# Kernel tuning notes

Hardware: AMD Instinct MI355X
Metric: run time of the kernel (lower is better)

The kernel has to match this reference:

```python
import jax, jax.numpy as jnp
import numpy as np

UNITS = [100, 80, 50, 30]
D_IN = 64


def _lstm_layer(x, Wx, Wh, b):
    # x: [B, T, D]; Wx: [D, 4u]; Wh: [u, 4u]; b: [4u]
    B = x.shape[0]
    u = Wh.shape[0]
    # precompute input contribution for all timesteps: [B, T, 4u]
    xg = jnp.einsum('btd,dg->btg', x, Wx) + b

    def step(carry, xg_t):
        h, c = carry
        g = xg_t + h @ Wh                      # [B, 4u]
        i, f, cbar, o = jnp.split(g, 4, axis=-1)
        i = jax.nn.sigmoid(i)
        f = jax.nn.sigmoid(f)
        o = jax.nn.sigmoid(o)
        c = f * c + i * jnp.tanh(cbar)
        h = o * jnp.tanh(c)
        return (h, c), h

    init = (jnp.zeros((B, u), x.dtype), jnp.zeros((B, u), x.dtype))
    (h_final, _), hs = jax.lax.scan(step, init, jnp.swapaxes(xg, 0, 1))
    return jnp.swapaxes(hs, 0, 1), h_final  # [B, T, u], [B, u]


def setup_inputs() -> dict:
    key = jax.random.key(0)
    ks = jax.random.split(key, 16)
    B, T = 256, 1024
    inp = {"sequence": jax.random.normal(ks[0], (B, T, D_IN), dtype=jnp.float32)}
    d_in = D_IN
    for li, u in enumerate(UNITS):
        s_x = 1.0 / np.sqrt(d_in)
        s_h = 1.0 / np.sqrt(u)
        inp[f"Wx{li}"] = jax.random.normal(ks[1 + 3 * li], (d_in, 4 * u), dtype=jnp.float32) * s_x
        inp[f"Wh{li}"] = jax.random.normal(ks[2 + 3 * li], (u, 4 * u), dtype=jnp.float32) * s_h
        inp[f"b{li}"] = jnp.zeros((4 * u,), dtype=jnp.float32)
        d_in = u
    inp["W_out"] = jax.random.normal(ks[13], (UNITS[-1], 1), dtype=jnp.float32) / np.sqrt(UNITS[-1])
    inp["b_out"] = jnp.zeros((1,), dtype=jnp.float32)
    return inp


def reference(sequence, Wx0, Wh0, b0, Wx1, Wh1, b1, Wx2, Wh2, b2, Wx3, Wh3, b3, W_out, b_out):
    # 4 stacked LSTM layers; dropout is identity at inference.
    x, _ = _lstm_layer(sequence, Wx0, Wh0, b0)   # [B, T, 100]
    x, _ = _lstm_layer(x, Wx1, Wh1, b1)          # [B, T, 80]
    x, _ = _lstm_layer(x, Wx2, Wh2, b2)          # [B, T, 50]
    _, h = _lstm_layer(x, Wx3, Wh3, b3)          # final state [B, 30]
    return h @ W_out + b_out                     # [B, 1]
```

## Files before the change

kernel.cpp:

```cpp
#include <hip/hip_runtime.h>


#define BATCH 256
#define TFULL 1024
#define TC    64
#define NCHUNK (TFULL / TC)
#define NDIAG  (NCHUNK + 3)

__device__ __forceinline__ float fast_rcp(float x) {
    return __builtin_amdgcn_rcpf(x);
}

__device__ __forceinline__ float tanh_fast(float x) {
    float e = __expf(-2.0f * fabsf(x));
    float r = fast_rcp(1.0f + e);
    return copysignf(fmaf(2.0f, r, -1.0f), x);
}

__device__ __forceinline__ void lds_barrier() {
    asm volatile("s_waitcnt lgkmcnt(0)\n\ts_barrier" ::: "memory");
}

template<int CTRL>
__device__ __forceinline__ float dpp_add(float v) {
    int t = __builtin_amdgcn_update_dpp(0, __float_as_int(v), CTRL, 0xF, 0xF, true);
    return v + __int_as_float(t);
}
template<int CTRL>
__device__ __forceinline__ float dpp_mov(float v) {
    int t = __builtin_amdgcn_update_dpp(0, __float_as_int(v), CTRL, 0xF, 0xF, true);
    return __int_as_float(t);
}

template<int K, int N>
__device__ __forceinline__ void gemm_body(
    const float* __restrict__ x, int batchStride,
    const float* __restrict__ Wx,
    const float* __restrict__ bias,
    float* __restrict__ out,
    int lid, float* __restrict__ smem)
{
    constexpr int K4   = (K + 3) / 4;
    constexpr int SLAB = 64 * 4 + 4;
    constexpr int GX   = (N + 63) / 64;

    float* s_A = smem;
    float* s_B = smem + K4 * SLAB;

    const int n0   = (lid % GX) * 64;
    const int row0 = (lid / GX) * 64;
    const int tid  = threadIdx.x;
    const int tx   = tid & 15;
    const int ty   = tid >> 4;

    if constexpr ((K % 4) == 0) {
        for (int i = tid; i < 64 * (K / 4); i += 256) {
            const int row = i / (K / 4);
            const int k4  = i % (K / 4);
            const int gr  = row0 + row;
            const int b   = gr >> 6;
            const int t   = gr & 63;
            float4 v = *(const float4*)(x + (size_t)b * batchStride + t * K + k4 * 4);
            *(float4*)(s_A + k4 * SLAB + row * 4) = v;
        }
    } else {
        for (int i = tid; i < 64 * K; i += 256) {
            const int row = i / K;
            const int k   = i % K;
            const int gr  = row0 + row;
            const int b   = gr >> 6;
            const int t   = gr & 63;
            s_A[(k >> 2) * SLAB + row * 4 + (k & 3)] =
                x[(size_t)b * batchStride + t * K + k];
        }
        constexpr int PAD = K4 * 4 - K;
        for (int i = tid; i < 64 * PAD; i += 256) {
            const int row = i / PAD;
            const int kk  = K + i % PAD;
            s_A[(kk >> 2) * SLAB + row * 4 + (kk & 3)] = 0.0f;
        }
    }

    for (int i = tid; i < K4 * 4 * 16; i += 256) {
        const int k  = i >> 4;
        const int c4 = i & 15;
        float4 v = {0.0f, 0.0f, 0.0f, 0.0f};
        if (k < K && n0 + c4 * 4 < N)
            v = *(const float4*)(Wx + (size_t)k * N + n0 + c4 * 4);
        *(float4*)(s_B + k * 64 + c4 * 4) = v;
    }
    __syncthreads();

    float acc[4][4];
#pragma unroll
    for (int r = 0; r < 4; ++r)
#pragma unroll
        for (int c = 0; c < 4; ++c) acc[r][c] = 0.0f;

    for (int k4 = 0; k4 < K4; ++k4) {
        float4 bv[4];
#pragma unroll
        for (int j = 0; j < 4; ++j)
            bv[j] = *(const float4*)(s_B + (k4 * 4 + j) * 64 + tx * 4);
#pragma unroll
        for (int r = 0; r < 4; ++r) {
            float4 av = *(const float4*)(s_A + k4 * SLAB + (ty + 16 * r) * 4);
#pragma unroll
            for (int c = 0; c < 4; ++c) {
                acc[r][c] = fmaf(av.x, ((const float*)&bv[0])[c], acc[r][c]);
                acc[r][c] = fmaf(av.y, ((const float*)&bv[1])[c], acc[r][c]);
                acc[r][c] = fmaf(av.z, ((const float*)&bv[2])[c], acc[r][c]);
                acc[r][c] = fmaf(av.w, ((const float*)&bv[3])[c], acc[r][c]);
            }
        }
    }

    if (n0 + tx * 4 < N) {
        float4 bb = *(const float4*)(bias + n0 + tx * 4);
#pragma unroll
        for (int r = 0; r < 4; ++r) {
            float4 o;
            o.x = acc[r][0] + bb.x;
            o.y = acc[r][1] + bb.y;
            o.z = acc[r][2] + bb.z;
            o.w = acc[r][3] + bb.w;
            *(float4*)(out + (size_t)(row0 + ty + 16 * r) * N + n0 + tx * 4) = o;
        }
    }
}

struct GemmArgs {
    const float *x0, *x1, *x2, *x3;
    float *o0, *o1, *o2, *o3;
    const float *Wx0, *bi0, *Wx1, *bi1, *Wx2, *bi2, *Wx3, *bi3;
    int off1, off2, off3;
};

__global__ __launch_bounds__(256, 2)
void xg_all(GemmArgs a)
{
    __shared__ __align__(16) float smem[12900];
    const int bid = blockIdx.x;
    if (bid < a.off1)
        gemm_body<64, 400>(a.x0, TFULL * 64, a.Wx0, a.bi0, a.o0, bid, smem);
    else if (bid < a.off2)
        gemm_body<100, 320>(a.x1, TC * 100, a.Wx1, a.bi1, a.o1, bid - a.off1, smem);
    else if (bid < a.off3)
        gemm_body<80, 200>(a.x2, TC * 80, a.Wx2, a.bi2, a.o2, bid - a.off2, smem);
    else
        gemm_body<50, 120>(a.x3, TC * 50, a.Wx3, a.bi3, a.o3, bid - a.off3, smem);
}

template<int U, int S, int BLOCK, bool LAST>
__device__ __forceinline__ void rec4_body(
    float* __restrict__ s_h,
    const float* __restrict__ xg,
    const float* __restrict__ Wh,
    float* __restrict__ xout,
    float* __restrict__ c_state,
    float* __restrict__ h_state,
    int first, int b,
    const float* __restrict__ Wout,
    const float* __restrict__ bout,
    float* __restrict__ dout)
{
    constexpr int G  = 4 * U;
    constexpr int HS = 4 * S;

    const int tid = threadIdx.x;
    const int u   = tid >> 2;
    const int s   = tid & 3;
    const bool act_th = (u < U);
    const int uu  = act_th ? u : 0;
    const bool wave_act = ((tid & ~63) < 4 * U);

    float w4[4][S];
#pragma unroll
    for (int g = 0; g < 4; ++g)
#pragma unroll
        for (int kk = 0; kk < S; ++kk) {
            const int k = s * S + kk;
            w4[g][kk] = (act_th && k < U) ? Wh[(size_t)k * G + g * U + uu] : 0.0f;
        }

    for (int i = tid; i < 2 * HS; i += BLOCK) s_h[i] = 0.0f;
    __syncthreads();
    if (tid < U) s_h[tid] = first ? 0.0f : h_state[b * U + tid];
    float c = first ? 0.0f : c_state[b * U + uu];
    __syncthreads();

    const float* xgp = xg + (size_t)b * TC * G + (s * U + uu);
    float xg0 = xgp[0];
    float xg1 = xgp[G];

    int cur = 0;
    float h = 0.0f, hprev = 0.0f;
    const bool is_t = (s == 2);

    for (int t = 0; t < TC; ++t, cur ^= 1) {
        if (wave_act) {
            const int tp = (t + 2 < TC) ? (t + 2) : (TC - 1);
            const float xg2 = xgp[(size_t)tp * G];

            if (!LAST) {
                if (act_th && s == 0 && t > 0)
                    xout[((size_t)b * TC + (t - 1)) * U + u] = hprev;
            }

            float a0 = 0.0f, a1 = 0.0f, a2 = 0.0f, a3 = 0.0f;
            const float* hs = s_h + cur * HS + s * S;
#pragma unroll
            for (int kk = 0; kk < S; kk += 4) {
                float4 v = *(const float4*)(hs + kk);
                a0 = fmaf(v.x, w4[0][kk + 0], a0);
                a0 = fmaf(v.y, w4[0][kk + 1], a0);
                a0 = fmaf(v.z, w4[0][kk + 2], a0);
                a0 = fmaf(v.w, w4[0][kk + 3], a0);
                a1 = fmaf(v.x, w4[1][kk + 0], a1);
                a1 = fmaf(v.y, w4[1][kk + 1], a1);
                a1 = fmaf(v.z, w4[1][kk + 2], a1);
                a1 = fmaf(v.w, w4[1][kk + 3], a1);
                a2 = fmaf(v.x, w4[2][kk + 0], a2);
                a2 = fmaf(v.y, w4[2][kk + 1], a2);
                a2 = fmaf(v.z, w4[2][kk + 2], a2);
                a2 = fmaf(v.w, w4[2][kk + 3], a2);
                a3 = fmaf(v.x, w4[3][kk + 0], a3);
                a3 = fmaf(v.y, w4[3][kk + 1], a3);
                a3 = fmaf(v.z, w4[3][kk + 2], a3);
                a3 = fmaf(v.w, w4[3][kk + 3], a3);
            }

            a0 = dpp_add<0xB1>(a0); a0 = dpp_add<0x4E>(a0);
            a1 = dpp_add<0xB1>(a1); a1 = dpp_add<0x4E>(a1);
            a2 = dpp_add<0xB1>(a2); a2 = dpp_add<0x4E>(a2);
            a3 = dpp_add<0xB1>(a3); a3 = dpp_add<0x4E>(a3);

            const float asum = (s == 0) ? a0 : (s == 1) ? a1 : (s == 2) ? a2 : a3;
            const float gs = asum + xg0;
            const float y  = is_t ? (-2.0f * fabsf(gs)) : (-gs);
            const float r  = fast_rcp(1.0f + __expf(y));
            const float v  = is_t ? copysignf(fmaf(2.0f, r, -1.0f), gs) : r;

            const float fi = dpp_mov<0x00>(v);
            const float ff = dpp_mov<0x55>(v);
            const float tc = dpp_mov<0xAA>(v);
            const float fo = dpp_mov<0xFF>(v);
            c = fmaf(ff, c, fi * tc);
            h = fo * tanh_fast(c);

            const int nxt = cur ^ 1;
            if (act_th && s == 0) s_h[nxt * HS + u] = h;
            hprev = h;
            xg0 = xg1; xg1 = xg2;
        }
        lds_barrier();
    }

    if (!LAST) {
        if (act_th && s == 0)
            xout[((size_t)b * TC + (TC - 1)) * U + u] = hprev;
    }
    if (act_th && s == 0) {
        c_state[b * U + u] = c;
        h_state[b * U + u] = h;
    }
    if (LAST && tid == 0) {
        float acc = bout[0];
#pragma unroll
        for (int k = 0; k < U; ++k) acc = fmaf(s_h[cur * HS + k], Wout[k], acc);
        dout[b] = acc;
    }
}

struct RecArgs {
    const float *xg0, *xg1, *xg2, *xg3;
    const float *Wh0, *Wh1, *Wh2, *Wh3;
    float *xc0, *xc1, *xc2;
    float *c0, *h0, *c1, *h1, *c2, *h2, *c3, *h3;
    const float *Wout, *bout;
    float *dout;
    int d;
};

__global__ __attribute__((amdgpu_flat_work_group_size(448, 448),
                          amdgpu_waves_per_eu(4, 8)))
void rec_all(RecArgs a)
{
    __shared__ __align__(16) float s_h[2 * 112];
    const int grp = blockIdx.x >> 8;
    const int b   = blockIdx.x & 255;
    const int j   = a.d - grp;
    if (j < 0 || j >= NCHUNK) return;
    const int first = (j == 0) ? 1 : 0;
    switch (grp) {
    case 0: rec4_body<100, 28, 448, false>(s_h, a.xg0, a.Wh0, a.xc0, a.c0, a.h0,
                                           first, b, nullptr, nullptr, nullptr); break;
    case 1: rec4_body< 80, 20, 448, false>(s_h, a.xg1, a.Wh1, a.xc1, a.c1, a.h1,
                                           first, b, nullptr, nullptr, nullptr); break;
    case 2: rec4_body< 50, 16, 448, false>(s_h, a.xg2, a.Wh2, a.xc2, a.c2, a.h2,
                                           first, b, nullptr, nullptr, nullptr); break;
    default: rec4_body< 30,  8, 448, true >(s_h, a.xg3, a.Wh3, nullptr, a.c3, a.h3,
                                           first, b, a.Wout, a.bout, a.dout); break;
    }
}

extern "C" void kernel_launch(void* const* d_in, const int* in_sizes, int n_in,
                              void* d_out, int out_size, void* d_ws, size_t ws_size,
                              hipStream_t stream)
{
    const float* seq  = (const float*)d_in[0];
    const float* Wx0  = (const float*)d_in[1];
    const float* Wh0  = (const float*)d_in[2];
    const float* b0   = (const float*)d_in[3];
    const float* Wx1  = (const float*)d_in[4];
    const float* Wh1  = (const float*)d_in[5];
    const float* b1   = (const float*)d_in[6];
    const float* Wx2  = (const float*)d_in[7];
    const float* Wh2  = (const float*)d_in[8];
    const float* b2   = (const float*)d_in[9];
    const float* Wx3  = (const float*)d_in[10];
    const float* Wh3  = (const float*)d_in[11];
    const float* b3   = (const float*)d_in[12];
    const float* Wout = (const float*)d_in[13];
    const float* bout = (const float*)d_in[14];
    float* out = (float*)d_out;

    float* ws  = (float*)d_ws;
    float* XG0 = ws;
    float* XG1 = XG0 + (size_t)BATCH * TC * 400;
    float* XG2 = XG1 + (size_t)BATCH * TC * 320;
    float* XG3 = XG2 + (size_t)BATCH * TC * 200;
    float* XC0 = XG3 + (size_t)BATCH * TC * 120;
    float* XC1 = XC0 + (size_t)BATCH * TC * 100;
    float* XC2 = XC1 + (size_t)BATCH * TC * 80;
    float* st  = XC2 + (size_t)BATCH * TC * 50;
    float* sc0 = st + 0 * 32768; float* sh0 = st + 1 * 32768;
    float* sc1 = st + 2 * 32768; float* sh1 = st + 3 * 32768;
    float* sc2 = st + 4 * 32768; float* sh2 = st + 5 * 32768;
    float* sc3 = st + 6 * 32768; float* sh3 = st + 7 * 32768;

    const int NB0 = 7 * 256, NB1 = 5 * 256, NB2 = 4 * 256, NB3 = 2 * 256;

    for (int d = 0; d < NDIAG; ++d) {
        GemmArgs ga;
        ga.x0 = nullptr; ga.x1 = nullptr; ga.x2 = nullptr; ga.x3 = nullptr;
        ga.o0 = XG0; ga.o1 = XG1; ga.o2 = XG2; ga.o3 = XG3;
        ga.Wx0 = Wx0; ga.bi0 = b0; ga.Wx1 = Wx1; ga.bi1 = b1;
        ga.Wx2 = Wx2; ga.bi2 = b2; ga.Wx3 = Wx3; ga.bi3 = b3;
        int nb = 0;
        if (d < NCHUNK)                { ga.x0 = seq + (size_t)d * TC * 64; nb += NB0; }
        ga.off1 = nb;
        if (d >= 1 && d - 1 < NCHUNK)  { ga.x1 = XC0; nb += NB1; }
        ga.off2 = nb;
        if (d >= 2 && d - 2 < NCHUNK)  { ga.x2 = XC1; nb += NB2; }
        ga.off3 = nb;
        if (d >= 3 && d - 3 < NCHUNK)  { ga.x3 = XC2; nb += NB3; }

        xg_all<<<dim3(nb), dim3(256), 0, stream>>>(ga);

        RecArgs ra;
        ra.xg0 = XG0; ra.xg1 = XG1; ra.xg2 = XG2; ra.xg3 = XG3;
        ra.Wh0 = Wh0; ra.Wh1 = Wh1; ra.Wh2 = Wh2; ra.Wh3 = Wh3;
        ra.xc0 = XC0; ra.xc1 = XC1; ra.xc2 = XC2;
        ra.c0 = sc0; ra.h0 = sh0; ra.c1 = sc1; ra.h1 = sh1;
        ra.c2 = sc2; ra.h2 = sh2; ra.c3 = sc3; ra.h3 = sh3;
        ra.Wout = Wout; ra.bout = bout; ra.dout = out;
        ra.d = d;

        rec_all<<<dim3(4 * 256), dim3(448), 0, stream>>>(ra);
    }
}
```

Baseline: 2.880 ms.

## Use fp16 MFMA for recurrent matmul, batching 16 sequences per block

The recurrent step moves from a per-sequence scalar FMA dot product (one block per batch element) to a 16-row MFMA tile. Each block now processes 16 sequences with Wh held in registers as fp16 fragments, and h is stored in LDS as fp16. The gate columns of the xg GEMM output are interleaved (i,f,c,o per unit) so each unit's four gates land in adjacent lanes for the DPP gather. The launch shrinks from 1024 blocks to 64 blocks of 512 threads. This trades precision (fp16 h and Wh) and parallelism (fewer blocks) for far fewer per-step instructions.

```diff
diff --git a/kernel.cpp b/kernel.cpp
--- a/kernel.cpp
+++ b/kernel.cpp
@@ -1,4 +1,5 @@
 #include <hip/hip_runtime.h>
+#include <hip/hip_fp16.h>
 
 
 #define BATCH 256
@@ -7,6 +8,9 @@
 #define NCHUNK (TFULL / TC)
 #define NDIAG  (NCHUNK + 3)
 
+typedef __attribute__((ext_vector_type(8))) _Float16 f16x8;
+typedef __attribute__((ext_vector_type(4))) float    f32x4;
+
 __device__ __forceinline__ float fast_rcp(float x) {
     return __builtin_amdgcn_rcpf(x);
 }
@@ -21,11 +25,6 @@
     asm volatile("s_waitcnt lgkmcnt(0)\n\ts_barrier" ::: "memory");
 }
 
-template<int CTRL>
-__device__ __forceinline__ float dpp_add(float v) {
-    int t = __builtin_amdgcn_update_dpp(0, __float_as_int(v), CTRL, 0xF, 0xF, true);
-    return v + __int_as_float(t);
-}
 template<int CTRL>
 __device__ __forceinline__ float dpp_mov(float v) {
     int t = __builtin_amdgcn_update_dpp(0, __float_as_int(v), CTRL, 0xF, 0xF, true);
@@ -43,6 +42,7 @@
     constexpr int K4   = (K + 3) / 4;
     constexpr int SLAB = 64 * 4 + 4;
     constexpr int GX   = (N + 63) / 64;
+    constexpr int U    = N / 4;
 
     float* s_A = smem;
     float* s_B = smem + K4 * SLAB;
@@ -84,9 +84,15 @@
     for (int i = tid; i < K4 * 4 * 16; i += 256) {
         const int k  = i >> 4;
         const int c4 = i & 15;
+        const int base = n0 + c4 * 4;
         float4 v = {0.0f, 0.0f, 0.0f, 0.0f};
-        if (k < K && n0 + c4 * 4 < N)
-            v = *(const float4*)(Wx + (size_t)k * N + n0 + c4 * 4);
+        if (k < K && base < N) {
+            const int q = base >> 2;
+            v.x = Wx[(size_t)k * N + 0 * U + q];
+            v.y = Wx[(size_t)k * N + 1 * U + q];
+            v.z = Wx[(size_t)k * N + 2 * U + q];
+            v.w = Wx[(size_t)k * N + 3 * U + q];
+        }
         *(float4*)(s_B + k * 64 + c4 * 4) = v;
     }
     __syncthreads();
@@ -116,7 +122,12 @@
     }
 
     if (n0 + tx * 4 < N) {
-        float4 bb = *(const float4*)(bias + n0 + tx * 4);
+        const int q = (n0 + tx * 4) >> 2;
+        float4 bb;
+        bb.x = bias[0 * U + q];
+        bb.y = bias[1 * U + q];
+        bb.z = bias[2 * U + q];
+        bb.w = bias[3 * U + q];
 #pragma unroll
         for (int r = 0; r < 4; ++r) {
             float4 o;
@@ -151,124 +162,162 @@
         gemm_body<50, 120>(a.x3, TC * 50, a.Wx3, a.bi3, a.o3, bid - a.off3, smem);
 }
 
-template<int U, int S, int BLOCK, bool LAST>
-__device__ __forceinline__ void rec4_body(
-    float* __restrict__ s_h,
+template<int U, int NT, int KT, bool LAST>
+__device__ __forceinline__ void recm_body(
     const float* __restrict__ xg,
     const float* __restrict__ Wh,
     float* __restrict__ xout,
     float* __restrict__ c_state,
     float* __restrict__ h_state,
-    int first, int b,
-    const float* __restrict__ Wout,
-    const float* __restrict__ bout,
-    float* __restrict__ dout)
+    const float* __restrict__ Wout, const float* __restrict__ bout,
+    float* __restrict__ dout,
+    int first, int b0, _Float16* __restrict__ s_h)
 {
     constexpr int G  = 4 * U;
-    constexpr int HS = 4 * S;
-
-    const int tid = threadIdx.x;
-    const int u   = tid >> 2;
-    const int s   = tid & 3;
-    const bool act_th = (u < U);
-    const int uu  = act_th ? u : 0;
-    const bool wave_act = ((tid & ~63) < 4 * U);
-
-    float w4[4][S];
-#pragma unroll
-    for (int g = 0; g < 4; ++g)
-#pragma unroll
-        for (int kk = 0; kk < S; ++kk) {
-            const int k = s * S + kk;
-            w4[g][kk] = (act_th && k < U) ? Wh[(size_t)k * G + g * U + uu] : 0.0f;
-        }
-
-    for (int i = tid; i < 2 * HS; i += BLOCK) s_h[i] = 0.0f;
+    constexpr int SH = 136;
+
+    const int tid  = threadIdx.x;
+    const int lane = tid & 63;
+    const int wave = tid >> 6;
+
+    const int ntS = (wave * NT) / 8;
+    const int ntE = ((wave + 1) * NT) / 8;
+
+    const int c0 = lane & 15;
+    const int rg = lane >> 4;
+    const int q  = (lane >> 2) & 3;
+    const int g  = lane & 3;
+    const bool is_t = (g == 2);
+    const bool wr   = (g == 0);
+
+    for (int i = tid; i < 2 * 16 * SH; i += 512) s_h[i] = (_Float16)0.0f;
     __syncthreads();
-    if (tid < U) s_h[tid] = first ? 0.0f : h_state[b * U + tid];
-    float c = first ? 0.0f : c_state[b * U + uu];
+    if (!first) {
+        for (int i = tid; i < 16 * U; i += 512) {
+            const int r = i / U, u = i % U;
+            s_h[r * SH + u] = (_Float16)h_state[(size_t)(b0 + r) * U + u];
+        }
+    }
     __syncthreads();
 
-    const float* xgp = xg + (size_t)b * TC * G + (s * U + uu);
-    float xg0 = xgp[0];
-    float xg1 = xgp[G];
+    f16x8 bf[4][KT];
+#pragma unroll
+    for (int nt = 0; nt < 4; ++nt) {
+        const int p  = (ntS + nt) * 16 + c0;
+        const int oc = (p & 3) * U + (p >> 2);
+        const bool pv = (ntS + nt < ntE) && (p < G);
+#pragma unroll
+        for (int kt = 0; kt < KT; ++kt) {
+#pragma unroll
+            for (int e = 0; e < 8; ++e) {
+                const int k = kt * 32 + rg * 8 + e;
+                const float w = (pv && k < U) ? Wh[(size_t)k * G + oc] : 0.0f;
+                bf[nt][kt][e] = (_Float16)w;
+            }
+        }
+    }
+
+    float cst[4][4];
+#pragma unroll
+    for (int nt = 0; nt < 4; ++nt) {
+        const int u = (ntS + nt) * 4 + q;
+        const bool uv = (ntS + nt < ntE) && (u < U);
+#pragma unroll
+        for (int j = 0; j < 4; ++j) {
+            const int r = rg * 4 + j;
+            cst[nt][j] = (!first && uv) ? c_state[(size_t)(b0 + r) * U + u] : 0.0f;
+        }
+    }
 
     int cur = 0;
-    float h = 0.0f, hprev = 0.0f;
-    const bool is_t = (s == 2);
-
-    for (int t = 0; t < TC; ++t, cur ^= 1) {
-        if (wave_act) {
-            const int tp = (t + 2 < TC) ? (t + 2) : (TC - 1);
-            const float xg2 = xgp[(size_t)tp * G];
-
-            if (!LAST) {
-                if (act_th && s == 0 && t > 0)
-                    xout[((size_t)b * TC + (t - 1)) * U + u] = hprev;
+    for (int t = 0; t < TC; ++t) {
+        float xv[4][4];
+#pragma unroll
+        for (int nt = 0; nt < 4; ++nt) {
+            if (ntS + nt < ntE) {
+                const int p  = (ntS + nt) * 16 + c0;
+                const bool pv = (p < G);
+#pragma unroll
+                for (int j = 0; j < 4; ++j) {
+                    const int r = rg * 4 + j;
+                    xv[nt][j] = pv ? xg[((size_t)(b0 + r) * TC + t) * G + p] : 0.0f;
+                }
+            } else {
+#pragma unroll
+                for (int j = 0; j < 4; ++j) xv[nt][j] = 0.0f;
             }
-
-            float a0 = 0.0f, a1 = 0.0f, a2 = 0.0f, a3 = 0.0f;
-            const float* hs = s_h + cur * HS + s * S;
-#pragma unroll
-            for (int kk = 0; kk < S; kk += 4) {
-                float4 v = *(const float4*)(hs + kk);
-                a0 = fmaf(v.x, w4[0][kk + 0], a0);
-                a0 = fmaf(v.y, w4[0][kk + 1], a0);
-                a0 = fmaf(v.z, w4[0][kk + 2], a0);
-                a0 = fmaf(v.w, w4[0][kk + 3], a0);
-                a1 = fmaf(v.x, w4[1][kk + 0], a1);
-                a1 = fmaf(v.y, w4[1][kk + 1], a1);
-                a1 = fmaf(v.z, w4[1][kk + 2], a1);
-                a1 = fmaf(v.w, w4[1][kk + 3], a1);
-                a2 = fmaf(v.x, w4[2][kk + 0], a2);
-                a2 = fmaf(v.y, w4[2][kk + 1], a2);
-                a2 = fmaf(v.z, w4[2][kk + 2], a2);
-                a2 = fmaf(v.w, w4[2][kk + 3], a2);
-                a3 = fmaf(v.x, w4[3][kk + 0], a3);
-                a3 = fmaf(v.y, w4[3][kk + 1], a3);
-                a3 = fmaf(v.z, w4[3][kk + 2], a3);
-                a3 = fmaf(v.w, w4[3][kk + 3], a3);
+        }
+
+        f16x8 af[KT];
+        const _Float16* hrow = s_h + cur * (16 * SH) + c0 * SH;
+#pragma unroll
+        for (int kt = 0; kt < KT; ++kt)
+            af[kt] = *(const f16x8*)(hrow + kt * 32 + rg * 8);
+
+        f32x4 acc[4];
+#pragma unroll
+        for (int nt = 0; nt < 4; ++nt) {
+            f32x4 a = {0.0f, 0.0f, 0.0f, 0.0f};
+            if (ntS + nt < ntE) {
+#pragma unroll
+                for (int kt = 0; kt < KT; ++kt)
+                    a = __builtin_amdgcn_mfma_f32_16x16x32_f16(af[kt], bf[nt][kt], a, 0, 0, 0);
             }
-
-            a0 = dpp_add<0xB1>(a0); a0 = dpp_add<0x4E>(a0);
-            a1 = dpp_add<0xB1>(a1); a1 = dpp_add<0x4E>(a1);
-            a2 = dpp_add<0xB1>(a2); a2 = dpp_add<0x4E>(a2);
-            a3 = dpp_add<0xB1>(a3); a3 = dpp_add<0x4E>(a3);
-
-            const float asum = (s == 0) ? a0 : (s == 1) ? a1 : (s == 2) ? a2 : a3;
-            const float gs = asum + xg0;
-            const float y  = is_t ? (-2.0f * fabsf(gs)) : (-gs);
-            const float r  = fast_rcp(1.0f + __expf(y));
-            const float v  = is_t ? copysignf(fmaf(2.0f, r, -1.0f), gs) : r;
-
-            const float fi = dpp_mov<0x00>(v);
-            const float ff = dpp_mov<0x55>(v);
-            const float tc = dpp_mov<0xAA>(v);
-            const float fo = dpp_mov<0xFF>(v);
-            c = fmaf(ff, c, fi * tc);
-            h = fo * tanh_fast(c);
-
-            const int nxt = cur ^ 1;
-            if (act_th && s == 0) s_h[nxt * HS + u] = h;
-            hprev = h;
-            xg0 = xg1; xg1 = xg2;
+            acc[nt] = a;
+        }
+
+#pragma unroll
+        for (int nt = 0; nt < 4; ++nt) {
+            if (ntS + nt < ntE) {
+                const int u = (ntS + nt) * 4 + q;
+                const bool uv = (u < U);
+#pragma unroll
+                for (int j = 0; j < 4; ++j) {
+                    const float gs = acc[nt][j] + xv[nt][j];
+                    const float y  = is_t ? (-2.0f * fabsf(gs)) : (-gs);
+                    const float rr = fast_rcp(1.0f + __expf(y));
+                    const float v  = is_t ? copysignf(fmaf(2.0f, rr, -1.0f), gs) : rr;
+                    const float fi = dpp_mov<0x00>(v);
+                    const float ff = dpp_mov<0x55>(v);
+                    const float tc = dpp_mov<0xAA>(v);
+                    const float fo = dpp_mov<0xFF>(v);
+                    const float c  = fmaf(ff, cst[nt][j], fi * tc);
+                    cst[nt][j] = c;
+                    const float h = fo * tanh_fast(c);
+                    if (wr && uv) {
+                        const int r = rg * 4 + j;
+                        s_h[(cur ^ 1) * (16 * SH) + r * SH + u] = (_Float16)h;
+                        if (!LAST)
+                            xout[((size_t)(b0 + r) * TC + t) * U + u] = h;
+                    }
+                }
+            }
         }
         lds_barrier();
-    }
-
-    if (!LAST) {
-        if (act_th && s == 0)
-            xout[((size_t)b * TC + (TC - 1)) * U + u] = hprev;
-    }
-    if (act_th && s == 0) {
-        c_state[b * U + u] = c;
-        h_state[b * U + u] = h;
-    }
-    if (LAST && tid == 0) {
-        float acc = bout[0];
-#pragma unroll
-        for (int k = 0; k < U; ++k) acc = fmaf(s_h[cur * HS + k], Wout[k], acc);
-        dout[b] = acc;
+        cur ^= 1;
+    }
+
+#pragma unroll
+    for (int nt = 0; nt < 4; ++nt) {
+        const int u = (ntS + nt) * 4 + q;
+        const bool uv = (ntS + nt < ntE) && (u < U);
+#pragma unroll
+        for (int j = 0; j < 4; ++j) {
+            if (wr && uv)
+                c_state[(size_t)(b0 + rg * 4 + j) * U + u] = cst[nt][j];
+        }
+    }
+    for (int i = tid; i < 16 * U; i += 512) {
+        const int r = i / U, u = i % U;
+        h_state[(size_t)(b0 + r) * U + u] = (float)s_h[cur * (16 * SH) + r * SH + u];
+    }
+    if (LAST) {
+        if (tid < 16) {
+            float acc = bout[0];
+            for (int u = 0; u < U; ++u)
+                acc = fmaf((float)s_h[cur * (16 * SH) + tid * SH + u], Wout[u], acc);
+            dout[b0 + tid] = acc;
+        }
     }
 }
 
@@ -282,25 +331,24 @@
     int d;
 };
 
-__global__ __attribute__((amdgpu_flat_work_group_size(448, 448),
-                          amdgpu_waves_per_eu(4, 8)))
+__global__ __launch_bounds__(512, 2)
 void rec_all(RecArgs a)
 {
-    __shared__ __align__(16) float s_h[2 * 112];
-    const int grp = blockIdx.x >> 8;
-    const int b   = blockIdx.x & 255;
+    __shared__ __align__(16) _Float16 s_h[2 * 16 * 136];
+    const int grp = blockIdx.x >> 4;
+    const int b0  = (blockIdx.x & 15) * 16;
     const int j   = a.d - grp;
     if (j < 0 || j >= NCHUNK) return;
     const int first = (j == 0) ? 1 : 0;
     switch (grp) {
-    case 0: rec4_body<100, 28, 448, false>(s_h, a.xg0, a.Wh0, a.xc0, a.c0, a.h0,
-                                           first, b, nullptr, nullptr, nullptr); break;
-    case 1: rec4_body< 80, 20, 448, false>(s_h, a.xg1, a.Wh1, a.xc1, a.c1, a.h1,
-                                           first, b, nullptr, nullptr, nullptr); break;
-    case 2: rec4_body< 50, 16, 448, false>(s_h, a.xg2, a.Wh2, a.xc2, a.c2, a.h2,
-                                           first, b, nullptr, nullptr, nullptr); break;
-    default: rec4_body< 30,  8, 448, true >(s_h, a.xg3, a.Wh3, nullptr, a.c3, a.h3,
-                                           first, b, a.Wout, a.bout, a.dout); break;
+    case 0: recm_body<100, 25, 4, false>(a.xg0, a.Wh0, a.xc0, a.c0, a.h0,
+                                         nullptr, nullptr, nullptr, first, b0, s_h); break;
+    case 1: recm_body< 80, 20, 3, false>(a.xg1, a.Wh1, a.xc1, a.c1, a.h1,
+                                         nullptr, nullptr, nullptr, first, b0, s_h); break;
+    case 2: recm_body< 50, 13, 2, false>(a.xg2, a.Wh2, a.xc2, a.c2, a.h2,
+                                         nullptr, nullptr, nullptr, first, b0, s_h); break;
+    default: recm_body< 30,  8, 1, true >(a.xg3, a.Wh3, nullptr, a.c3, a.h3,
+                                         a.Wout, a.bout, a.dout, first, b0, s_h); break;
     }
 }
 
@@ -367,6 +415,6 @@
         ra.Wout = Wout; ra.bout = bout; ra.dout = out;
         ra.d = d;
 
-        rec_all<<<dim3(4 * 256), dim3(448), 0, stream>>>(ra);
-    }
-}
+        rec_all<<<dim3(64), dim3(512), 0, stream>>>(ra);
+    }
+}
```

After: 4.641 ms. +61.1%, slower.
